# Kernel optimization log

Hardware: AMD Instinct MI355X
Metric: run time of the kernel (lower is better)

## Reference

```python
import jax, jax.numpy as jnp
import numpy as np

B, IN, H = 8192, 512, 512


def _binarize(w):
    # sign() forward with straight-through gradient (ebnn Binarize)
    return w + jax.lax.stop_gradient(jnp.sign(w) - w)


def setup_inputs() -> dict:
    key = jax.random.key(0)
    ks = jax.random.split(key, 7)
    stdv = 1.0 / np.sqrt(H)
    return {
        "x": jax.random.normal(ks[0], (B, IN), jnp.float32),
        "hx": jax.random.normal(ks[1], (B, H), jnp.float32),
        "cx": jax.random.normal(ks[2], (B, H), jnp.float32),
        "W_ih": jax.random.uniform(ks[3], (4 * H, IN), jnp.float32, -stdv, stdv),
        "W_hh": jax.random.uniform(ks[4], (4 * H, H), jnp.float32, -stdv, stdv),
        "bias_ih": jax.random.uniform(ks[5], (4 * H,), jnp.float32, -stdv, stdv),
        "bias_hh": jax.random.uniform(ks[6], (4 * H,), jnp.float32, -stdv, stdv),
    }


def reference(x, hx, cx, W_ih, W_hh, bias_ih, bias_hh):
    # gates: [B, 4H] = x @ sign(W_ih)^T + b_ih + hx @ sign(W_hh)^T + b_hh
    gates = (jnp.einsum("bi,gi->bg", x, _binarize(W_ih)) + bias_ih
             + jnp.einsum("bh,gh->bg", hx, _binarize(W_hh)) + bias_hh)
    ingate, forgetgate, cellgate, outgate = jnp.split(gates, 4, axis=1)
    cy = jax.nn.sigmoid(forgetgate) * cx + jax.nn.sigmoid(ingate) * jnp.tanh(cellgate)
    hy = jax.nn.sigmoid(outgate) * jnp.tanh(cy)
    return (hy, cy)
```

## Files before the change

kernel.cpp:

```cpp
#include <hip/hip_runtime.h>
#include <hip/hip_bf16.h>
#include <stdint.h>


typedef __attribute__((ext_vector_type(4))) int int4x;
typedef __attribute__((ext_vector_type(4))) float float4x;

#define B_DIM 8192
#define H_DIM 512

__device__ __forceinline__ float bf2f(uint16_t u) {
  return __uint_as_float(((uint32_t)u) << 16);
}
__device__ __forceinline__ uint16_t f2bf(float f) {
  uint32_t u = __float_as_uint(f);
  return (uint16_t)((u + 0x7FFFu + ((u >> 16) & 1u)) >> 16);
}
__device__ __forceinline__ float sigm(float x) { return 1.0f / (1.0f + __expf(-x)); }
__device__ __forceinline__ float tanh_f(float x) { return 2.0f / (1.0f + __expf(-2.0f * x)) - 1.0f; }

__device__ __forceinline__ int detect_f32(const void* x) {
  const int l = threadIdx.x & 63;
  uint32_t wrd = ((const uint32_t*)x)[l];
  uint32_t e0 = (wrd >> 7) & 0xFFu, e1 = (wrd >> 23) & 0xFFu;
  return __ballot(e0 > 0x85u || e1 > 0x85u) != 0ull;
}

__device__ __forceinline__ void quant4(const float* v, uint32_t* hi4, uint32_t* lo4) {
  uint32_t h = 0, lo = 0;
#pragma unroll
  for (int j = 0; j < 4; ++j) {
    float c = fminf(fmaxf(v[j], -8.0f), 8.0f);
    int xf = __float2int_rn(c * 4096.0f);
    xf = xf > 32639 ? 32639 : xf;
    xf = xf < -32768 ? -32768 : xf;
    const int lb = (xf << 24) >> 24;
    const int hb = (xf - lb) >> 8;
    lo |= ((uint32_t)lb & 0xFFu) << (8 * j);
    h |= ((uint32_t)hb & 0xFFu) << (8 * j);
  }
  *hi4 = h;
  *lo4 = lo;
}

__global__ __launch_bounds__(256) void prep_kernel(
    const void* __restrict__ x, const void* __restrict__ hx,
    const void* __restrict__ w_ih, const void* __restrict__ w_hh,
    int8_t* __restrict__ Xhi, int8_t* __restrict__ Xlo, int8_t* __restrict__ Bp) {
  __shared__ alignas(16) char lsc[33280];
  const int isF32 = detect_f32(x);
  const int t = threadIdx.x;
  const int w = t >> 6, l = t & 63;
  const int isX = blockIdx.x < 512;
  const int grp = isX ? blockIdx.x : (blockIdx.x - 512);

#pragma unroll
  for (int rr = 0; rr < 4; ++rr) {
    const int r = w * 4 + rr;
    long rowbase;
    if (isX) rowbase = (long)(grp * 16 + r) * 512;
    else     rowbase = (long)((grp & 3) * 512 + (grp >> 2) * 16 + r) * 512;
#pragma unroll
    for (int src = 0; src < 2; ++src) {
      const void* sp_ = isX ? (src ? hx : x) : (src ? w_hh : w_ih);
#pragma unroll
      for (int q = 0; q < 2; ++q) {
        const int k = src * 512 + q * 256 + l * 4;
        float v[4];
        if (isF32) {
          float4x f = *(const float4x*)((const float*)sp_ + rowbase + q * 256 + l * 4);
          v[0] = f[0]; v[1] = f[1]; v[2] = f[2]; v[3] = f[3];
        } else {
          const uint16_t* s = (const uint16_t*)sp_ + rowbase + q * 256 + l * 4;
#pragma unroll
          for (int j = 0; j < 4; ++j) v[j] = bf2f(s[j]);
        }
        if (isX) {
          uint32_t h4, lo4;
          quant4(v, &h4, &lo4);
          *(uint32_t*)(lsc + r * 1040 + k) = h4;
          *(uint32_t*)(lsc + 16640 + r * 1040 + k) = lo4;
        } else {
          uint32_t s4 = 0;
#pragma unroll
          for (int j = 0; j < 4; ++j) {
            const int sv = v[j] > 0.f ? 1 : (v[j] < 0.f ? -1 : 0);
            s4 |= ((uint32_t)sv & 0xFFu) << (8 * j);
          }
          *(uint32_t*)(lsc + r * 1040 + k) = s4;
        }
      }
    }
  }
  __syncthreads();
  const int kt = t >> 4, quad = (t >> 2) & 3, rb = (t & 3) * 4;
  const int loff = kt * 64 + quad * 16;
  if (isX) {
    int4x h[4], lo[4];
#pragma unroll
    for (int i = 0; i < 4; ++i) {
      h[i] = *(const int4x*)(lsc + (rb + i) * 1040 + loff);
      lo[i] = *(const int4x*)(lsc + 16640 + (rb + i) * 1040 + loff);
    }
    int4x* dh = (int4x*)(Xhi + (long)grp * 16384 + t * 64);
    int4x* dl = (int4x*)(Xlo + (long)grp * 16384 + t * 64);
#pragma unroll
    for (int i = 0; i < 4; ++i) { dh[i] = h[i]; dl[i] = lo[i]; }
  } else {
    int4x s[4];
#pragma unroll
    for (int i = 0; i < 4; ++i)
      s[i] = *(const int4x*)(lsc + (rb + i) * 1040 + loff);
    int4x* db = (int4x*)(Bp + (long)grp * 16384 + t * 64);
#pragma unroll
    for (int i = 0; i < 4; ++i) db[i] = s[i];
  }
}

__global__ __launch_bounds__(256, 3) void blstm_gemm_kernel(
    const int8_t* __restrict__ Xhi, const int8_t* __restrict__ Xlo,
    const int8_t* __restrict__ Bp, const void* __restrict__ b_ih,
    const void* __restrict__ b_hh, const void* __restrict__ cx,
    const void* __restrict__ xdet, void* __restrict__ out) {
  __shared__ alignas(16) char lds[16384];
  const int tid = threadIdx.x;
  const int l = tid & 63, w = tid >> 6;
  const int lrow = l & 15, lq = l >> 4;
  const int wy = w >> 1, wx = w & 1;
  const int isF32 = detect_f32(xdet);
  const int bid = blockIdx.x;
  const int by = (bid & 7) * 16 + ((bid >> 3) & 15);
  const int bx = bid >> 7;

  const int8_t* ap[4];
#pragma unroll
  for (int mt = 0; mt < 2; ++mt) {
    const long t16 = ((long)(by * 4 + wy * 2 + mt) << 14) + l * 16;
    ap[mt] = Xhi + t16;
    ap[2 + mt] = Xlo + t16;
  }
  const int8_t* bp[2];
  int dof[2];
#pragma unroll
  for (int i = 0; i < 2; ++i) {
    const int c = w * 2 + i;
    bp[i] = Bp + ((long)(bx * 8 + c) << 14) + l * 16;
    dof[i] = c * 1024 + l * 16;
  }

  int4x acch[2][4], accl[2][4];
#pragma unroll
  for (int mt = 0; mt < 2; ++mt)
#pragma unroll
    for (int g = 0; g < 4; ++g) {
      acch[mt][g] = (int4x){0, 0, 0, 0};
      accl[mt][g] = (int4x){0, 0, 0, 0};
    }

  int4x bst[2][2];
  int4x afr[2][4];
#pragma unroll
  for (int i = 0; i < 2; ++i) { bst[0][i] = *(const int4x*)bp[i]; bp[i] += 1024; }
#pragma unroll
  for (int i = 0; i < 4; ++i) { afr[0][i] = *(const int4x*)ap[i]; ap[i] += 1024; }
#pragma unroll
  for (int i = 0; i < 2; ++i) *(int4x*)(lds + dof[i]) = bst[0][i];
  asm volatile("s_waitcnt lgkmcnt(0)\n\ts_barrier" ::: "memory");

#pragma unroll
  for (int ks = 0; ks < 16; ++ks) {
    const int cur = ks & 1, nxt = cur ^ 1;
    if (ks < 15) {
#pragma unroll
      for (int i = 0; i < 2; ++i) { bst[nxt][i] = *(const int4x*)bp[i]; bp[i] += 1024; }
#pragma unroll
      for (int i = 0; i < 4; ++i) { afr[nxt][i] = *(const int4x*)ap[i]; ap[i] += 1024; }
    }
    int4x b[4];
#pragma unroll
    for (int g = 0; g < 4; ++g)
      b[g] = *(const int4x*)(lds + cur * 8192 + (wx * 4 + g) * 1024 + l * 16);
#pragma unroll
    for (int mt = 0; mt < 2; ++mt)
#pragma unroll
      for (int g = 0; g < 4; ++g) {
        acch[mt][g] = __builtin_amdgcn_mfma_i32_16x16x64_i8(afr[cur][mt], b[g], acch[mt][g], 0, 0, 0);
        accl[mt][g] = __builtin_amdgcn_mfma_i32_16x16x64_i8(afr[cur][2 + mt], b[g], accl[mt][g], 0, 0, 0);
      }
    if (ks < 15) {
#pragma unroll
      for (int i = 0; i < 2; ++i) *(int4x*)(lds + nxt * 8192 + dof[i]) = bst[nxt][i];
      asm volatile("s_waitcnt lgkmcnt(0)\n\ts_barrier" ::: "memory");
    }
  }

  const long CYo = (long)B_DIM * H_DIM;
  const int c = bx * 32 + wx * 16 + lrow;
  float biasv[4];
#pragma unroll
  for (int g = 0; g < 4; ++g) {
    if (isF32)
      biasv[g] = ((const float*)b_ih)[g * 512 + c] + ((const float*)b_hh)[g * 512 + c];
    else
      biasv[g] = bf2f(((const uint16_t*)b_ih)[g * 512 + c]) + bf2f(((const uint16_t*)b_hh)[g * 512 + c]);
  }
  float* outF = (float*)out;
  uint16_t* outB = (uint16_t*)out;
#pragma unroll
  for (int mt = 0; mt < 2; ++mt) {
#pragma unroll
    for (int r = 0; r < 4; ++r) {
      const int row = by * 64 + wy * 32 + mt * 16 + lq * 4 + r;
      const long cidx = (long)row * H_DIM + c;
      float vg[4];
#pragma unroll
      for (int g = 0; g < 4; ++g)
        vg[g] = fmaf((float)acch[mt][g][r], 0.0625f,
                     fmaf((float)accl[mt][g][r], 2.44140625e-4f, biasv[g]));
      const float cxv = isF32 ? ((const float*)cx)[cidx] : bf2f(((const uint16_t*)cx)[cidx]);
      const float ig = sigm(vg[0]), fg = sigm(vg[1]), og = sigm(vg[3]);
      const float cg = tanh_f(vg[2]);
      const float cy = fg * cxv + ig * cg;
      const float hy = og * tanh_f(cy);
      if (isF32) {
        outF[cidx] = hy;
        outF[CYo + cidx] = cy;
      } else {
        outB[cidx] = f2bf(hy);
        outB[CYo + cidx] = f2bf(cy);
      }
    }
  }
}

extern "C" void kernel_launch(void* const* d_in, const int* in_sizes, int n_in,
                              void* d_out, int out_size, void* d_ws, size_t ws_size,
                              hipStream_t stream) {
  const void* x = d_in[0];
  const void* hx = d_in[1];
  const void* cx = d_in[2];
  const void* W_ih = d_in[3];
  const void* W_hh = d_in[4];
  const void* b_ih = d_in[5];
  const void* b_hh = d_in[6];
  char* ws = (char*)d_ws;
  int8_t* Xhi = (int8_t*)ws;
  int8_t* Xlo = (int8_t*)(ws + 8388608);
  int8_t* Bp = (int8_t*)(ws + 16777216);

  prep_kernel<<<640, 256, 0, stream>>>(x, hx, W_ih, W_hh, Xhi, Xlo, Bp);
  blstm_gemm_kernel<<<2048, 256, 0, stream>>>(Xhi, Xlo, Bp, b_ih, b_hh, cx, x, d_out);
}
```

Measured before the change: 154.6 us.

## Enlarge GEMM block tile to 256 rows with half-K B staging in LDS

Reworks the int8 MFMA GEMM into 512-thread blocks that each compute 256 batch rows by 32 hidden columns. Each wave now holds 4 row tiles instead of 2, so every B fragment read from LDS is reused more. B is staged in two bulk half-K loads into 64 KB of LDS instead of being double-buffered every k-step, which removes 14 per-step barriers. MFMA sections are wrapped in s_setprio. The cost is fewer blocks (512), more accumulator registers and more LDS per block, which may lower occupancy and leave a full load-then-barrier stall at the midpoint.

```diff
diff --git a/kernel.cpp b/kernel.cpp
--- a/kernel.cpp
+++ b/kernel.cpp
@@ -117,81 +117,81 @@
   }
 }
 
-__global__ __launch_bounds__(256, 3) void blstm_gemm_kernel(
+__global__ __launch_bounds__(512, 2) void blstm_gemm_kernel(
     const int8_t* __restrict__ Xhi, const int8_t* __restrict__ Xlo,
     const int8_t* __restrict__ Bp, const void* __restrict__ b_ih,
     const void* __restrict__ b_hh, const void* __restrict__ cx,
     const void* __restrict__ xdet, void* __restrict__ out) {
-  __shared__ alignas(16) char lds[16384];
+  __shared__ alignas(16) char lds[65536];
   const int tid = threadIdx.x;
   const int l = tid & 63, w = tid >> 6;
   const int lrow = l & 15, lq = l >> 4;
   const int wy = w >> 1, wx = w & 1;
   const int isF32 = detect_f32(xdet);
   const int bid = blockIdx.x;
-  const int by = (bid & 7) * 16 + ((bid >> 3) & 15);
-  const int bx = bid >> 7;
-
-  const int8_t* ap[4];
-#pragma unroll
-  for (int mt = 0; mt < 2; ++mt) {
-    const long t16 = ((long)(by * 4 + wy * 2 + mt) << 14) + l * 16;
-    ap[mt] = Xhi + t16;
-    ap[2 + mt] = Xlo + t16;
-  }
-  const int8_t* bp[2];
-  int dof[2];
-#pragma unroll
-  for (int i = 0; i < 2; ++i) {
-    const int c = w * 2 + i;
-    bp[i] = Bp + ((long)(bx * 8 + c) << 14) + l * 16;
-    dof[i] = c * 1024 + l * 16;
-  }
-
-  int4x acch[2][4], accl[2][4];
-#pragma unroll
-  for (int mt = 0; mt < 2; ++mt)
+  const int rt = (bid & 7) * 4 + (bid >> 7);
+  const int bx = (bid >> 3) & 15;
+
+  const int8_t* aph[4];
+  const int8_t* apl[4];
+#pragma unroll
+  for (int mt = 0; mt < 4; ++mt) {
+    const long off = ((long)(rt * 16 + wy * 4 + mt) << 14) + l * 16;
+    aph[mt] = Xhi + off;
+    apl[mt] = Xlo + off;
+  }
+  const int8_t* bsrc = Bp + ((long)(bx * 8) << 14) + tid * 16;
+
+  int4x acch[4][4], accl[4][4];
+#pragma unroll
+  for (int mt = 0; mt < 4; ++mt)
 #pragma unroll
     for (int g = 0; g < 4; ++g) {
       acch[mt][g] = (int4x){0, 0, 0, 0};
       accl[mt][g] = (int4x){0, 0, 0, 0};
     }
 
-  int4x bst[2][2];
-  int4x afr[2][4];
-#pragma unroll
-  for (int i = 0; i < 2; ++i) { bst[0][i] = *(const int4x*)bp[i]; bp[i] += 1024; }
-#pragma unroll
-  for (int i = 0; i < 4; ++i) { afr[0][i] = *(const int4x*)ap[i]; ap[i] += 1024; }
-#pragma unroll
-  for (int i = 0; i < 2; ++i) *(int4x*)(lds + dof[i]) = bst[0][i];
+  int4x ah[2][4], al[2][4];
+#pragma unroll
+  for (int mt = 0; mt < 4; ++mt) {
+    ah[0][mt] = *(const int4x*)aph[mt]; aph[mt] += 1024;
+    al[0][mt] = *(const int4x*)apl[mt]; apl[mt] += 1024;
+  }
+#pragma unroll
+  for (int g = 0; g < 8; ++g)
+    *(int4x*)(lds + g * 8192 + tid * 16) = *(const int4x*)(bsrc + g * 16384);
   asm volatile("s_waitcnt lgkmcnt(0)\n\ts_barrier" ::: "memory");
 
 #pragma unroll
   for (int ks = 0; ks < 16; ++ks) {
     const int cur = ks & 1, nxt = cur ^ 1;
+    if (ks == 8) {
+      asm volatile("s_waitcnt lgkmcnt(0)\n\ts_barrier" ::: "memory");
+#pragma unroll
+      for (int g = 0; g < 8; ++g)
+        *(int4x*)(lds + g * 8192 + tid * 16) = *(const int4x*)(bsrc + g * 16384 + 8192);
+      asm volatile("s_waitcnt lgkmcnt(0)\n\ts_barrier" ::: "memory");
+    }
     if (ks < 15) {
 #pragma unroll
-      for (int i = 0; i < 2; ++i) { bst[nxt][i] = *(const int4x*)bp[i]; bp[i] += 1024; }
-#pragma unroll
-      for (int i = 0; i < 4; ++i) { afr[nxt][i] = *(const int4x*)ap[i]; ap[i] += 1024; }
+      for (int mt = 0; mt < 4; ++mt) {
+        ah[nxt][mt] = *(const int4x*)aph[mt]; aph[mt] += 1024;
+        al[nxt][mt] = *(const int4x*)apl[mt]; apl[mt] += 1024;
+      }
     }
     int4x b[4];
 #pragma unroll
     for (int g = 0; g < 4; ++g)
-      b[g] = *(const int4x*)(lds + cur * 8192 + (wx * 4 + g) * 1024 + l * 16);
-#pragma unroll
-    for (int mt = 0; mt < 2; ++mt)
+      b[g] = *(const int4x*)(lds + (wx * 4 + g) * 8192 + (ks & 7) * 1024 + l * 16);
+    __builtin_amdgcn_s_setprio(1);
+#pragma unroll
+    for (int mt = 0; mt < 4; ++mt)
 #pragma unroll
       for (int g = 0; g < 4; ++g) {
-        acch[mt][g] = __builtin_amdgcn_mfma_i32_16x16x64_i8(afr[cur][mt], b[g], acch[mt][g], 0, 0, 0);
-        accl[mt][g] = __builtin_amdgcn_mfma_i32_16x16x64_i8(afr[cur][2 + mt], b[g], accl[mt][g], 0, 0, 0);
-      }
-    if (ks < 15) {
-#pragma unroll
-      for (int i = 0; i < 2; ++i) *(int4x*)(lds + nxt * 8192 + dof[i]) = bst[nxt][i];
-      asm volatile("s_waitcnt lgkmcnt(0)\n\ts_barrier" ::: "memory");
-    }
+        acch[mt][g] = __builtin_amdgcn_mfma_i32_16x16x64_i8(ah[cur][mt], b[g], acch[mt][g], 0, 0, 0);
+        accl[mt][g] = __builtin_amdgcn_mfma_i32_16x16x64_i8(al[cur][mt], b[g], accl[mt][g], 0, 0, 0);
+      }
+    __builtin_amdgcn_s_setprio(0);
   }
 
   const long CYo = (long)B_DIM * H_DIM;
@@ -207,10 +207,10 @@
   float* outF = (float*)out;
   uint16_t* outB = (uint16_t*)out;
 #pragma unroll
-  for (int mt = 0; mt < 2; ++mt) {
+  for (int mt = 0; mt < 4; ++mt) {
 #pragma unroll
     for (int r = 0; r < 4; ++r) {
-      const int row = by * 64 + wy * 32 + mt * 16 + lq * 4 + r;
+      const int row = rt * 256 + wy * 64 + mt * 16 + lq * 4 + r;
       const long cidx = (long)row * H_DIM + c;
       float vg[4];
 #pragma unroll
@@ -249,5 +249,5 @@
   int8_t* Bp = (int8_t*)(ws + 16777216);
 
   prep_kernel<<<640, 256, 0, stream>>>(x, hx, W_ih, W_hh, Xhi, Xlo, Bp);
-  blstm_gemm_kernel<<<2048, 256, 0, stream>>>(Xhi, Xlo, Bp, b_ih, b_hh, cx, x, d_out);
-}
+  blstm_gemm_kernel<<<512, 512, 0, stream>>>(Xhi, Xlo, Bp, b_ih, b_hh, cx, x, d_out);
+}
```

New measurement: 172.7 us. +11.7%, slower.
